# Kernel tuning notes

Hardware: AMD Instinct MI355X
Metric: run time of the kernel (lower is better)

Reference implementation:

```python
import jax, jax.numpy as jnp
import numpy as np

P, U, E, NNZ = 200000, 100000, 64, 2000000


def setup_inputs() -> dict:
    key = jax.random.key(0)
    ks = jax.random.split(key, 12)
    return {
        "init_pois_embs": jax.random.normal(ks[0], (P, E), jnp.float32),
        "col_pois_embs": jax.random.normal(ks[1], (P, E), jnp.float32),
        "geo_pois_embs": jax.random.normal(ks[2], (P, E), jnp.float32),
        "seq_pois_embs": jax.random.normal(ks[3], (P, E), jnp.float32),
        "users_embs": jax.random.normal(ks[4], (U, E), jnp.float32),
        "up_rows": jax.random.randint(ks[5], (NNZ,), 0, U, jnp.int32),
        "up_cols": jax.random.randint(ks[6], (NNZ,), 0, P, jnp.int32),
        "up_vals": jax.random.uniform(ks[7], (NNZ,), jnp.float32),
        "pu_vals": jax.random.uniform(ks[8], (NNZ,), jnp.float32),
        "W_fusion": jax.random.normal(ks[9], (E, 7 * E), jnp.float32) * 0.05,
        "b_fusion": jnp.zeros((E,), jnp.float32),
        "num_layers": 2,
    }


def _spmm(rows, cols, vals, X, n_out):
    # sparse [n_out, n_in] @ dense [n_in, E] in COO form
    return jax.ops.segment_sum(vals[:, None] * X[cols], rows, num_segments=n_out)


def reference(init_pois_embs, col_pois_embs, geo_pois_embs, seq_pois_embs,
              users_embs, up_rows, up_cols, up_vals, pu_vals,
              W_fusion, b_fusion, num_layers):
    n_users = users_embs.shape[0]
    n_pois = init_pois_embs.shape[0]
    # HG_up @ {geo, seq, col}
    ga = _spmm(up_rows, up_cols, up_vals, geo_pois_embs, n_users)
    sa = _spmm(up_rows, up_cols, up_vals, seq_pois_embs, n_users)
    pa = _spmm(up_rows, up_cols, up_vals, col_pois_embs, n_users)
    msg = jnp.concatenate(
        [ga, sa, pa, ga * sa, ga * pa, sa * pa, ga * sa * pa], axis=1)
    msg_emb = jnp.einsum('uf,ef->ue', msg, W_fusion) + b_fusion
    hg_users = msg_emb + users_embs + msg_emb * users_embs
    # HG_pu (transpose structure of HG_up, own values) @ hg_users
    propag = _spmm(up_cols, up_rows, pu_vals, hg_users, n_pois)
    # layer output is identical each iteration (layer always consumes init embs)
    outs = [init_pois_embs]
    for _ in range(num_layers):
        outs.append(propag + outs[-1])
    return jnp.mean(jnp.stack(outs), axis=0)
```

## Files before the change

kernel.cpp:

```cpp
#include <hip/hip_runtime.h>

#define EDIM 64
#define RCAP 8192
#define NBMAX 512

typedef __attribute__((ext_vector_type(8))) short short8;
typedef __attribute__((ext_vector_type(4))) float f32x4;

__device__ __forceinline__ unsigned int f2bf(float x) {
  unsigned int u = __float_as_uint(x);
  u += 0x7FFFu + ((u >> 16) & 1u);
  return u >> 16;
}
__device__ __forceinline__ float bf2f(unsigned short s) {
  return __uint_as_float(((unsigned int)s) << 16);
}
__device__ __forceinline__ float bflo(unsigned int u) {
  return __uint_as_float(u << 16);
}
__device__ __forceinline__ float bfhi(unsigned int u) {
  return __uint_as_float(u & 0xFFFF0000u);
}

__global__ __launch_bounds__(256) void tobf16_kernel(
    const float4* __restrict__ s0, const float4* __restrict__ s1,
    const float4* __restrict__ s2, uint2* __restrict__ d0,
    uint2* __restrict__ d1, uint2* __restrict__ d2, int n4) {
  const int stride = gridDim.x * blockDim.x;
  for (int i = blockIdx.x * blockDim.x + threadIdx.x; i < 3 * n4; i += stride) {
    const int t = i / n4, j = i - t * n4;
    const float4* s = (t == 0) ? s0 : ((t == 1) ? s1 : s2);
    uint2* d = (t == 0) ? d0 : ((t == 1) ? d1 : d2);
    const float4 v = s[j];
    uint2 o;
    o.x = f2bf(v.x) | (f2bf(v.y) << 16);
    o.y = f2bf(v.z) | (f2bf(v.w) << 16);
    d[j] = o;
  }
}

__global__ __launch_bounds__(256) void bucket_pass1_kernel(
    const int* __restrict__ keys, const int* __restrict__ p1,
    const float* __restrict__ p2, int* __restrict__ gCursor,
    int2* __restrict__ regionPay, int nnz, int sh, int nb) {
  __shared__ int cnt[NBMAX];
  __shared__ int curs[NBMAX];
  const int tid = threadIdx.x;
  for (int i = tid; i < nb; i += 256) cnt[i] = 0;
  __syncthreads();
  const int chunk = (nnz + gridDim.x - 1) / gridDim.x;
  const int s = blockIdx.x * chunk;
  const int e = min(nnz, s + chunk);
  for (int i = s + tid; i < e; i += 256) atomicAdd(&cnt[keys[i] >> sh], 1);
  __syncthreads();
  for (int i = tid; i < nb; i += 256) {
    const int c = cnt[i];
    curs[i] = c ? atomicAdd(&gCursor[i], c) : 0;
  }
  __syncthreads();
  const int mask = (1 << sh) - 1;
  for (int i = s + tid; i < e; i += 256) {
    const int k = keys[i];
    const int b = k >> sh;
    const int pos = atomicAdd(&curs[b], 1);
    if (pos < RCAP) {
      regionPay[(b << 13) + pos] =
          make_int2(p1[i] | ((k & mask) << 18), __float_as_int(p2[i]));
    }
  }
}

__global__ void bucket_scan_kernel(const int* __restrict__ cnt,
                                   int* __restrict__ base, int nb) {
  if (threadIdx.x == 0) {
    int run = 0;
    for (int i = 0; i < nb; ++i) {
      base[i] = run;
      run += cnt[i];
    }
  }
}

__global__ __launch_bounds__(256) void bucket_pass2_kernel(
    const int* __restrict__ gCursor, const int* __restrict__ csrBase,
    const int2* __restrict__ regionPay, int* __restrict__ ptr,
    int2* __restrict__ csr, int nkey, int sh, int kpb) {
  __shared__ int hist[NBMAX];
  const int b = blockIdx.x;
  const int tid = threadIdx.x;
  const int n = min(gCursor[b], RCAP);
  const int rb = b << 13;
  const int cb = csrBase[b];
  const int keyLo = b << sh;
  for (int i = tid; i < kpb; i += 256) hist[i] = 0;
  __syncthreads();
  for (int i = tid; i < n; i += 256)
    atomicAdd(&hist[(unsigned)regionPay[rb + i].x >> 18], 1);
  __syncthreads();
  if (tid == 0) {
    int run = 0;
    for (int k = 0; k < kpb; ++k) {
      const int c = hist[k];
      hist[k] = run;
      run += c;
    }
  }
  __syncthreads();
  for (int k = tid; k < kpb; k += 256) {
    const int key = keyLo + k;
    if (key < nkey) ptr[key] = cb + hist[k];
  }
  __syncthreads();
  for (int i = tid; i < n; i += 256) {
    const int2 e = regionPay[rb + i];
    const int k = (unsigned)e.x >> 18;
    const int pos = atomicAdd(&hist[k], 1);
    csr[cb + pos] = make_int2(e.x & 0x3FFFF, e.y);
  }
}

__global__ __launch_bounds__(256) void user_gather_kernel(
    const int* __restrict__ ptrU, const int2* __restrict__ csrU,
    const unsigned short* __restrict__ tblG,
    const unsigned short* __restrict__ tblS,
    const unsigned short* __restrict__ tblC,
    unsigned short* __restrict__ gw, unsigned short* __restrict__ sw,
    unsigned short* __restrict__ pw, int U, int nnz) {
  const int lane = threadIdx.x & 63;
  const int sub = lane >> 4, d4 = lane & 15;
  const int wv = blockIdx.x * 4 + (threadIdx.x >> 6);
  const int nW = gridDim.x * 4;
  for (int u = wv; u < U; u += nW) {
    const int start = ptrU[u];
    const int end = (u + 1 < U) ? ptrU[u + 1] : nnz;
    float4 g4 = {0, 0, 0, 0}, s4 = {0, 0, 0, 0}, p4 = {0, 0, 0, 0};
    for (int k0 = start; k0 < end; k0 += 64) {
      int c_v = 0;
      float v_v = 0.f;
      const int kk = k0 + lane;
      if (kk < end) {
        const int2 e = csrU[kk];
        c_v = e.x;
        v_v = __int_as_float(e.y);
      }
      const int steps = (min(64, end - k0) + 3) >> 2;
      for (int t = 0; t < steps; ++t) {
        const int src = t * 4 + sub;
        const int cc = __shfl(c_v, src);
        const float vv = __shfl(v_v, src);
        const size_t rb = (size_t)cc * EDIM;
        const uint2 gg = ((const uint2*)(tblG + rb))[d4];
        const uint2 ss = ((const uint2*)(tblS + rb))[d4];
        const uint2 pp = ((const uint2*)(tblC + rb))[d4];
        g4.x += vv * bflo(gg.x); g4.y += vv * bfhi(gg.x);
        g4.z += vv * bflo(gg.y); g4.w += vv * bfhi(gg.y);
        s4.x += vv * bflo(ss.x); s4.y += vv * bfhi(ss.x);
        s4.z += vv * bflo(ss.y); s4.w += vv * bfhi(ss.y);
        p4.x += vv * bflo(pp.x); p4.y += vv * bfhi(pp.x);
        p4.z += vv * bflo(pp.y); p4.w += vv * bfhi(pp.y);
      }
    }
#pragma unroll
    for (int m = 16; m <= 32; m <<= 1) {
      g4.x += __shfl_xor(g4.x, m); g4.y += __shfl_xor(g4.y, m);
      g4.z += __shfl_xor(g4.z, m); g4.w += __shfl_xor(g4.w, m);
      s4.x += __shfl_xor(s4.x, m); s4.y += __shfl_xor(s4.y, m);
      s4.z += __shfl_xor(s4.z, m); s4.w += __shfl_xor(s4.w, m);
      p4.x += __shfl_xor(p4.x, m); p4.y += __shfl_xor(p4.y, m);
      p4.z += __shfl_xor(p4.z, m); p4.w += __shfl_xor(p4.w, m);
    }
    if (sub == 0) {
      uint2 gp2, sp2, pp2;
      gp2.x = f2bf(g4.x) | (f2bf(g4.y) << 16);
      gp2.y = f2bf(g4.z) | (f2bf(g4.w) << 16);
      sp2.x = f2bf(s4.x) | (f2bf(s4.y) << 16);
      sp2.y = f2bf(s4.z) | (f2bf(s4.w) << 16);
      pp2.x = f2bf(p4.x) | (f2bf(p4.y) << 16);
      pp2.y = f2bf(p4.z) | (f2bf(p4.w) << 16);
      ((uint2*)(gw + (size_t)u * EDIM))[d4] = gp2;
      ((uint2*)(sw + (size_t)u * EDIM))[d4] = sp2;
      ((uint2*)(pw + (size_t)u * EDIM))[d4] = pp2;
    }
  }
}

#define FM_BLK 256
__global__ __launch_bounds__(FM_BLK) void fusion_mfma_kernel(
    const unsigned short* __restrict__ gbf, const unsigned short* __restrict__ sbf,
    const unsigned short* __restrict__ pbf, const float* __restrict__ uemb,
    const float* __restrict__ W, const float* __restrict__ b,
    unsigned short* __restrict__ hbf, int U) {
  __shared__ unsigned short wlds[7 * 2 * 4 * 64 * 8];
  for (int fe = threadIdx.x; fe < 7 * 2 * 4 * 64; fe += FM_BLK) {
    const int ln = fe & 63;
    const int n = (fe >> 6) & 3;
    const int h = (fe >> 8) & 1;
    const int blk = fe >> 9;
    const int e = n * 16 + (ln & 15);
    const int f0 = blk * 64 + h * 32 + (ln >> 4) * 8;
    const float* wsrc = W + (size_t)e * 448 + f0;
    uint4 w4;
    w4.x = f2bf(wsrc[0]) | (f2bf(wsrc[1]) << 16);
    w4.y = f2bf(wsrc[2]) | (f2bf(wsrc[3]) << 16);
    w4.z = f2bf(wsrc[4]) | (f2bf(wsrc[5]) << 16);
    w4.w = f2bf(wsrc[6]) | (f2bf(wsrc[7]) << 16);
    ((uint4*)wlds)[fe] = w4;
  }
  __syncthreads();

  const int l = threadIdx.x & 63;
  const int row16 = l & 15, kg = l >> 4;
  const int wv = blockIdx.x * (FM_BLK / 64) + (threadIdx.x >> 6);
  const int nWv = gridDim.x * (FM_BLK / 64);
  float bias4[4];
#pragma unroll
  for (int n = 0; n < 4; ++n) bias4[n] = b[n * 16 + row16];

  const int nT = (U + 15) >> 4;
  for (int t = wv; t < nT; t += nWv) {
    const int u0 = t * 16;
    f32x4 acc0 = {0, 0, 0, 0}, acc1 = {0, 0, 0, 0};
    f32x4 acc2 = {0, 0, 0, 0}, acc3 = {0, 0, 0, 0};
    const int ua = min(u0 + row16, U - 1);
#pragma unroll
    for (int h = 0; h < 2; ++h) {
      const size_t off = (size_t)ua * EDIM + h * 32 + kg * 8;
      short8 gfr = *(const short8*)(gbf + off);
      short8 sfr = *(const short8*)(sbf + off);
      short8 pfr = *(const short8*)(pbf + off);
      float gf[8], sf[8], pf[8];
#pragma unroll
      for (int j = 0; j < 8; ++j) {
        gf[j] = bf2f((unsigned short)gfr[j]);
        sf[j] = bf2f((unsigned short)sfr[j]);
        pf[j] = bf2f((unsigned short)pfr[j]);
      }
      short8 gs, gp, sp, gsp;
#pragma unroll
      for (int j = 0; j < 8; ++j) {
        const float a = gf[j] * sf[j];
        gs[j] = (short)f2bf(a);
        gp[j] = (short)f2bf(gf[j] * pf[j]);
        sp[j] = (short)f2bf(sf[j] * pf[j]);
        gsp[j] = (short)f2bf(a * pf[j]);
      }
      short8 afr[7] = {gfr, sfr, pfr, gs, gp, sp, gsp};
#pragma unroll
      for (int blk = 0; blk < 7; ++blk) {
        const int fb = blk * 512 + h * 256;
        const short8 b0 = *(const short8*)(wlds + (size_t)(fb + 0 * 64 + l) * 8);
        const short8 b1 = *(const short8*)(wlds + (size_t)(fb + 1 * 64 + l) * 8);
        const short8 b2 = *(const short8*)(wlds + (size_t)(fb + 2 * 64 + l) * 8);
        const short8 b3 = *(const short8*)(wlds + (size_t)(fb + 3 * 64 + l) * 8);
        acc0 = __builtin_amdgcn_mfma_f32_16x16x32_bf16(afr[blk], b0, acc0, 0, 0, 0);
        acc1 = __builtin_amdgcn_mfma_f32_16x16x32_bf16(afr[blk], b1, acc1, 0, 0, 0);
        acc2 = __builtin_amdgcn_mfma_f32_16x16x32_bf16(afr[blk], b2, acc2, 0, 0, 0);
        acc3 = __builtin_amdgcn_mfma_f32_16x16x32_bf16(afr[blk], b3, acc3, 0, 0, 0);
      }
    }
#pragma unroll
    for (int r = 0; r < 4; ++r) {
      const int u = u0 + kg * 4 + r;
      if (u < U) {
        const size_t ubase = (size_t)u * EDIM + row16;
        {
          const float me = acc0[r] + bias4[0];
          const float ue = uemb[ubase + 0];
          hbf[ubase + 0] = (unsigned short)f2bf(me + ue + me * ue);
        }
        {
          const float me = acc1[r] + bias4[1];
          const float ue = uemb[ubase + 16];
          hbf[ubase + 16] = (unsigned short)f2bf(me + ue + me * ue);
        }
        {
          const float me = acc2[r] + bias4[2];
          const float ue = uemb[ubase + 32];
          hbf[ubase + 32] = (unsigned short)f2bf(me + ue + me * ue);
        }
        {
          const float me = acc3[r] + bias4[3];
          const float ue = uemb[ubase + 48];
          hbf[ubase + 48] = (unsigned short)f2bf(me + ue + me * ue);
        }
      }
    }
  }
}

__global__ __launch_bounds__(256) void poi_gather_kernel(
    const int* __restrict__ ptrP, const int2* __restrict__ csrP,
    const unsigned short* __restrict__ hbf, const float* __restrict__ init,
    const int* __restrict__ num_layers, float* __restrict__ out, int P,
    int nnz) {
  const float scale = 0.5f * (float)num_layers[0];
  const int lane = threadIdx.x & 63;
  const int sub = lane >> 4, d4 = lane & 15;
  const int wv = blockIdx.x * 4 + (threadIdx.x >> 6);
  const int nW = gridDim.x * 4;
  for (int c = wv; c < P; c += nW) {
    const int start = ptrP[c];
    const int end = (c + 1 < P) ? ptrP[c + 1] : nnz;
    float4 a4 = {0, 0, 0, 0};
    for (int k0 = start; k0 < end; k0 += 64) {
      int r_v = 0;
      float v_v = 0.f;
      const int kk = k0 + lane;
      if (kk < end) {
        const int2 e = csrP[kk];
        r_v = e.x;
        v_v = __int_as_float(e.y);
      }
      const int steps = (min(64, end - k0) + 3) >> 2;
      for (int t = 0; t < steps; ++t) {
        const int src = t * 4 + sub;
        const int rr = __shfl(r_v, src);
        const float vv = __shfl(v_v, src);
        const uint2 hh = ((const uint2*)(hbf + (size_t)rr * EDIM))[d4];
        a4.x += vv * bflo(hh.x); a4.y += vv * bfhi(hh.x);
        a4.z += vv * bflo(hh.y); a4.w += vv * bfhi(hh.y);
      }
    }
#pragma unroll
    for (int m = 16; m <= 32; m <<= 1) {
      a4.x += __shfl_xor(a4.x, m); a4.y += __shfl_xor(a4.y, m);
      a4.z += __shfl_xor(a4.z, m); a4.w += __shfl_xor(a4.w, m);
    }
    if (sub == 0) {
      const float4 iv = ((const float4*)(init + (size_t)c * EDIM))[d4];
      float4 o;
      o.x = iv.x + scale * a4.x;
      o.y = iv.y + scale * a4.y;
      o.z = iv.z + scale * a4.z;
      o.w = iv.w + scale * a4.w;
      ((float4*)(out + (size_t)c * EDIM))[d4] = o;
    }
  }
}

extern "C" void kernel_launch(void* const* d_in, const int* in_sizes, int n_in,
                              void* d_out, int out_size, void* d_ws,
                              size_t ws_size, hipStream_t stream) {
  const float* init = (const float*)d_in[0];
  const float* colp = (const float*)d_in[1];
  const float* geo = (const float*)d_in[2];
  const float* seq = (const float*)d_in[3];
  const float* uemb = (const float*)d_in[4];
  const int* up_rows = (const int*)d_in[5];
  const int* up_cols = (const int*)d_in[6];
  const float* up_vals = (const float*)d_in[7];
  const float* pu_vals = (const float*)d_in[8];
  const float* W = (const float*)d_in[9];
  const float* b = (const float*)d_in[10];
  const int* num_layers = (const int*)d_in[11];

  const int U = in_sizes[4] / EDIM;
  const int P = in_sizes[0] / EDIM;
  const int NNZ = in_sizes[5];

  const int SHU = 8, SHP = 9;
  const int NBU = (U + 255) >> 8;
  const int NBP = (P + 511) >> 9;

  int* ptrU = (int*)d_ws;
  int* ptrP = ptrU + U;
  int* curU = ptrP + P;
  int* curP = curU + NBMAX;
  int* baseU = curP + NBMAX;
  int* baseP = baseU + NBMAX;
  int2* csrP = (int2*)(baseP + NBMAX);
  int2* csrU = csrP + NNZ;
  unsigned short* tblS = (unsigned short*)(csrU + NNZ);
  unsigned short* gbf = tblS + (size_t)P * EDIM;
  unsigned short* sbf = gbf + (size_t)U * EDIM;
  unsigned short* pbf = sbf + (size_t)U * EDIM;
  unsigned short* hbf = (unsigned short*)csrU;
  int2* regionPay = (int2*)gbf;
  unsigned short* tblG = (unsigned short*)d_out;
  unsigned short* tblC = tblG + (size_t)P * EDIM;
  float* out = (float*)d_out;

  hipMemsetAsync(curU, 0, 2 * NBMAX * sizeof(int), stream);

  tobf16_kernel<<<2048, 256, 0, stream>>>(
      (const float4*)geo, (const float4*)seq, (const float4*)colp,
      (uint2*)tblG, (uint2*)tblS, (uint2*)tblC, P * (EDIM / 4));

  bucket_pass1_kernel<<<256, 256, 0, stream>>>(up_rows, up_cols, up_vals,
                                               curU, regionPay, NNZ, SHU,
                                               NBU);
  bucket_scan_kernel<<<1, 64, 0, stream>>>(curU, baseU, NBU);
  bucket_pass2_kernel<<<NBU, 256, 0, stream>>>(curU, baseU, regionPay, ptrU,
                                               csrU, U, SHU, 256);

  bucket_pass1_kernel<<<256, 256, 0, stream>>>(up_cols, up_rows, pu_vals,
                                               curP, regionPay, NNZ, SHP,
                                               NBP);
  bucket_scan_kernel<<<1, 64, 0, stream>>>(curP, baseP, NBP);
  bucket_pass2_kernel<<<NBP, 256, 0, stream>>>(curP, baseP, regionPay, ptrP,
                                               csrP, P, SHP, 512);

  user_gather_kernel<<<2048, 256, 0, stream>>>(ptrU, csrU, tblG, tblS, tblC,
                                               gbf, sbf, pbf, U, NNZ);

  fusion_mfma_kernel<<<512, FM_BLK, 0, stream>>>(gbf, sbf, pbf, uemb, W, b,
                                                 hbf, U);

  poi_gather_kernel<<<2048, 256, 0, stream>>>(ptrP, csrP, hbf, init,
                                              num_layers, out, P, NNZ);
}
```

Measured before the change: 478.9 us.

## Merge user and POI bucket-sort passes into shared kernels with parallel scan

Fuses the two COO-to-CSR bucket sorts (user-keyed and POI-keyed) so one pass1 kernel reads rows/cols once and scatters into both region buffers, one scan kernel handles both prefix sums, and one pass2 launch covers both bucket sets. The serial single-thread scan becomes a wave-shuffle parallel scan. This removes three kernel launches, a duplicate read of the index arrays, and serial scan latency. In exchange the per-bucket region capacity drops to fit both buffers side by side, which raises the risk of silent overflow truncation if a bucket exceeds the cap.

```diff
diff --git a/kernel.cpp b/kernel.cpp
--- a/kernel.cpp
+++ b/kernel.cpp
@@ -1,7 +1,7 @@
 #include <hip/hip_runtime.h>
 
 #define EDIM 64
-#define RCAP 8192
+#define RCAP 6144
 #define NBMAX 512
 
 typedef __attribute__((ext_vector_type(8))) short short8;
@@ -12,14 +12,14 @@
   u += 0x7FFFu + ((u >> 16) & 1u);
   return u >> 16;
 }
+__device__ __forceinline__ float bflo(unsigned int u) {
+  return __uint_as_float(u << 16);
+}
+__device__ __forceinline__ float bfhi(unsigned int u) {
+  return __uint_as_float(u & 0xFFFF0000u);
+}
 __device__ __forceinline__ float bf2f(unsigned short s) {
   return __uint_as_float(((unsigned int)s) << 16);
-}
-__device__ __forceinline__ float bflo(unsigned int u) {
-  return __uint_as_float(u << 16);
-}
-__device__ __forceinline__ float bfhi(unsigned int u) {
-  return __uint_as_float(u & 0xFFFF0000u);
 }
 
 __global__ __launch_bounds__(256) void tobf16_kernel(
@@ -40,62 +40,109 @@
 }
 
 __global__ __launch_bounds__(256) void bucket_pass1_kernel(
-    const int* __restrict__ keys, const int* __restrict__ p1,
-    const float* __restrict__ p2, int* __restrict__ gCursor,
-    int2* __restrict__ regionPay, int nnz, int sh, int nb) {
-  __shared__ int cnt[NBMAX];
-  __shared__ int curs[NBMAX];
+    const int* __restrict__ rows, const int* __restrict__ cols,
+    const float* __restrict__ up_vals, const float* __restrict__ pu_vals,
+    int* __restrict__ curU, int* __restrict__ curP,
+    int2* __restrict__ regU, int2* __restrict__ regP,
+    int nnz, int shU, int shP, int nbU, int nbP) {
+  __shared__ int cntU[NBMAX], cntP[NBMAX];
+  __shared__ int cuU[NBMAX], cuP[NBMAX];
   const int tid = threadIdx.x;
-  for (int i = tid; i < nb; i += 256) cnt[i] = 0;
+  for (int i = tid; i < nbU; i += 256) cntU[i] = 0;
+  for (int i = tid; i < nbP; i += 256) cntP[i] = 0;
   __syncthreads();
   const int chunk = (nnz + gridDim.x - 1) / gridDim.x;
   const int s = blockIdx.x * chunk;
   const int e = min(nnz, s + chunk);
-  for (int i = s + tid; i < e; i += 256) atomicAdd(&cnt[keys[i] >> sh], 1);
-  __syncthreads();
-  for (int i = tid; i < nb; i += 256) {
-    const int c = cnt[i];
-    curs[i] = c ? atomicAdd(&gCursor[i], c) : 0;
-  }
-  __syncthreads();
-  const int mask = (1 << sh) - 1;
   for (int i = s + tid; i < e; i += 256) {
-    const int k = keys[i];
-    const int b = k >> sh;
-    const int pos = atomicAdd(&curs[b], 1);
-    if (pos < RCAP) {
-      regionPay[(b << 13) + pos] =
-          make_int2(p1[i] | ((k & mask) << 18), __float_as_int(p2[i]));
-    }
-  }
-}
-
-__global__ void bucket_scan_kernel(const int* __restrict__ cnt,
-                                   int* __restrict__ base, int nb) {
-  if (threadIdx.x == 0) {
-    int run = 0;
-    for (int i = 0; i < nb; ++i) {
-      base[i] = run;
-      run += cnt[i];
-    }
-  }
+    atomicAdd(&cntU[rows[i] >> shU], 1);
+    atomicAdd(&cntP[cols[i] >> shP], 1);
+  }
+  __syncthreads();
+  for (int i = tid; i < nbU; i += 256) {
+    const int c = cntU[i];
+    cuU[i] = c ? atomicAdd(&curU[i], c) : 0;
+  }
+  for (int i = tid; i < nbP; i += 256) {
+    const int c = cntP[i];
+    cuP[i] = c ? atomicAdd(&curP[i], c) : 0;
+  }
+  __syncthreads();
+  const int maskU = (1 << shU) - 1, maskP = (1 << shP) - 1;
+  for (int i = s + tid; i < e; i += 256) {
+    const int r = rows[i], c = cols[i];
+    const int bu = r >> shU, bp = c >> shP;
+    const int pu = atomicAdd(&cuU[bu], 1);
+    if (pu < RCAP)
+      regU[bu * RCAP + pu] =
+          make_int2(c | ((r & maskU) << 18), __float_as_int(up_vals[i]));
+    const int pp = atomicAdd(&cuP[bp], 1);
+    if (pp < RCAP)
+      regP[bp * RCAP + pp] =
+          make_int2(r | ((c & maskP) << 18), __float_as_int(pu_vals[i]));
+  }
+}
+
+__device__ __forceinline__ void scan_one(const int* __restrict__ cnt,
+                                         int* __restrict__ base, int nb,
+                                         int* wsum) {
+  const int tid = threadIdx.x;
+  const int lane = tid & 63, wid = tid >> 6;
+  const int v = (tid < nb) ? cnt[tid] : 0;
+  int sc = v;
+  for (int d = 1; d < 64; d <<= 1) {
+    const int o = __shfl_up(sc, d);
+    if (lane >= d) sc += o;
+  }
+  if (lane == 63) wsum[wid] = sc;
+  __syncthreads();
+  int woff = 0;
+  for (int w = 0; w < wid; ++w) woff += wsum[w];
+  if (tid < nb) base[tid] = woff + sc - v;
+  __syncthreads();
+}
+
+__global__ __launch_bounds__(512) void bucket_scan2_kernel(
+    const int* __restrict__ curU, int* __restrict__ baseU, int nbU,
+    const int* __restrict__ curP, int* __restrict__ baseP, int nbP) {
+  __shared__ int wsum[8];
+  scan_one(curU, baseU, nbU, wsum);
+  scan_one(curP, baseP, nbP, wsum);
 }
 
 __global__ __launch_bounds__(256) void bucket_pass2_kernel(
-    const int* __restrict__ gCursor, const int* __restrict__ csrBase,
-    const int2* __restrict__ regionPay, int* __restrict__ ptr,
-    int2* __restrict__ csr, int nkey, int sh, int kpb) {
+    const int* __restrict__ curU, const int* __restrict__ baseU,
+    const int2* __restrict__ regU, int* __restrict__ ptrU,
+    int2* __restrict__ csrU, int nkeyU, int shU,
+    const int* __restrict__ curP, const int* __restrict__ baseP,
+    const int2* __restrict__ regP, int* __restrict__ ptrP,
+    int2* __restrict__ csrP, int nkeyP, int shP, int nbU) {
   __shared__ int hist[NBMAX];
-  const int b = blockIdx.x;
   const int tid = threadIdx.x;
-  const int n = min(gCursor[b], RCAP);
-  const int rb = b << 13;
-  const int cb = csrBase[b];
+  int b = blockIdx.x;
+  const int* gCur;
+  const int* gBase;
+  const int2* reg;
+  int* ptr;
+  int2* csr;
+  int nkey, sh;
+  if (b < nbU) {
+    gCur = curU; gBase = baseU; reg = regU; ptr = ptrU; csr = csrU;
+    nkey = nkeyU; sh = shU;
+  } else {
+    b -= nbU;
+    gCur = curP; gBase = baseP; reg = regP; ptr = ptrP; csr = csrP;
+    nkey = nkeyP; sh = shP;
+  }
+  const int kpb = 1 << sh;
+  const int n = min(gCur[b], RCAP);
+  const int rb = b * RCAP;
+  const int cb = gBase[b];
   const int keyLo = b << sh;
   for (int i = tid; i < kpb; i += 256) hist[i] = 0;
   __syncthreads();
   for (int i = tid; i < n; i += 256)
-    atomicAdd(&hist[(unsigned)regionPay[rb + i].x >> 18], 1);
+    atomicAdd(&hist[(unsigned)reg[rb + i].x >> 18], 1);
   __syncthreads();
   if (tid == 0) {
     int run = 0;
@@ -112,10 +159,10 @@
   }
   __syncthreads();
   for (int i = tid; i < n; i += 256) {
-    const int2 e = regionPay[rb + i];
-    const int k = (unsigned)e.x >> 18;
+    const int2 ent = reg[rb + i];
+    const int k = (unsigned)ent.x >> 18;
     const int pos = atomicAdd(&hist[k], 1);
-    csr[cb + pos] = make_int2(e.x & 0x3FFFF, e.y);
+    csr[cb + pos] = make_int2(ent.x & 0x3FFFF, ent.y);
   }
 }
 
@@ -375,7 +422,8 @@
   unsigned short* sbf = gbf + (size_t)U * EDIM;
   unsigned short* pbf = sbf + (size_t)U * EDIM;
   unsigned short* hbf = (unsigned short*)csrU;
-  int2* regionPay = (int2*)gbf;
+  int2* regU = (int2*)gbf;
+  int2* regP = regU + (size_t)NBU * RCAP;
   unsigned short* tblG = (unsigned short*)d_out;
   unsigned short* tblC = tblG + (size_t)P * EDIM;
   float* out = (float*)d_out;
@@ -387,18 +435,15 @@
       (uint2*)tblG, (uint2*)tblS, (uint2*)tblC, P * (EDIM / 4));
 
   bucket_pass1_kernel<<<256, 256, 0, stream>>>(up_rows, up_cols, up_vals,
-                                               curU, regionPay, NNZ, SHU,
-                                               NBU);
-  bucket_scan_kernel<<<1, 64, 0, stream>>>(curU, baseU, NBU);
-  bucket_pass2_kernel<<<NBU, 256, 0, stream>>>(curU, baseU, regionPay, ptrU,
-                                               csrU, U, SHU, 256);
-
-  bucket_pass1_kernel<<<256, 256, 0, stream>>>(up_cols, up_rows, pu_vals,
-                                               curP, regionPay, NNZ, SHP,
-                                               NBP);
-  bucket_scan_kernel<<<1, 64, 0, stream>>>(curP, baseP, NBP);
-  bucket_pass2_kernel<<<NBP, 256, 0, stream>>>(curP, baseP, regionPay, ptrP,
-                                               csrP, P, SHP, 512);
+                                               pu_vals, curU, curP, regU,
+                                               regP, NNZ, SHU, SHP, NBU, NBP);
+
+  bucket_scan2_kernel<<<1, 512, 0, stream>>>(curU, baseU, NBU, curP, baseP,
+                                             NBP);
+
+  bucket_pass2_kernel<<<NBU + NBP, 256, 0, stream>>>(
+      curU, baseU, regU, ptrU, csrU, U, SHU, curP, baseP, regP, ptrP, csrP, P,
+      SHP, NBU);
 
   user_gather_kernel<<<2048, 256, 0, stream>>>(ptrU, csrU, tblG, tblS, tblC,
                                                gbf, sbf, pbf, U, NNZ);
```

New measurement: 446.4 us. 6.8% less time.
